# Optimization experiments

Measured on AMD Instinct MI355X. Metric: run time of the kernel, lower is better.

## Reference

```python
import jax, jax.numpy as jnp
import numpy as np

T, V, E, K, D, H, BERT = 4, 4096, 4096, 32, 8, 16, 768
CAT = H + BERT  # 784, second LSTM input size


def setup_inputs() -> dict:
    key = jax.random.key(0)
    ks = jax.random.split(key, 24)
    n = lambda k, s: jax.random.normal(k, s, dtype=jnp.float32) * 0.02
    return dict(
        prices=jax.random.normal(ks[0], (T, V, 1), dtype=jnp.float32),
        node_embs=jax.random.normal(ks[1], (T, E, BERT), dtype=jnp.float32),
        he_members=jax.random.randint(ks[2], (T, E, K), 0, V),
        vert_edges=jax.random.randint(ks[3], (T, V, D), 0, E),
        Wih_p=n(ks[4], (4 * H, 1)), Whh_p=n(ks[5], (4 * H, H)),
        bih_p=n(ks[6], (4 * H,)), bhh_p=n(ks[7], (4 * H,)),
        Wih_m=n(ks[8], (4 * H, CAT)), Whh_m=n(ks[9], (4 * H, H)),
        bih_m=n(ks[10], (4 * H,)), bhh_m=n(ks[11], (4 * H,)),
        vc_trans_w=n(ks[12], (K, K, H)), vc_trans_b=n(ks[13], (K, K)),
        vc_conv_w=n(ks[14], (K,)), vc_conv_b=n(ks[15], (1,)),
        ec_w1=n(ks[16], (CAT // 4, CAT)), ec_b1=n(ks[17], (CAT // 4,)),
        ec_w2=n(ks[18], (1, CAT // 4)), ec_b2=n(ks[19], (1,)),
        attn_in=n(ks[20], (H, H)), attn_out=n(ks[21], (H, 2 * H)),
        fc_w=n(ks[22], (2, H)), fc_b=n(ks[23], (2,)),
    )


def _lstm(x, Wih, Whh, bih, bhh):
    # x: (T, B, in) -> hidden states (T, B, H); PyTorch gate order i,f,g,o
    h0 = jnp.zeros((x.shape[1], Whh.shape[1]), x.dtype)
    b = bih + bhh

    def step(carry, xt):
        h, c = carry
        g = xt @ Wih.T + h @ Whh.T + b
        i, f, gg, o = jnp.split(g, 4, axis=-1)
        c = jax.nn.sigmoid(f) * c + jax.nn.sigmoid(i) * jnp.tanh(gg)
        h = jax.nn.sigmoid(o) * jnp.tanh(c)
        return (h, c), h

    _, hs = jax.lax.scan(step, (h0, h0), x)
    return hs


def reference(prices, node_embs, he_members, vert_edges,
              Wih_p, Whh_p, bih_p, bhh_p,
              Wih_m, Whh_m, bih_m, bhh_m,
              vc_trans_w, vc_trans_b, vc_conv_w, vc_conv_b,
              ec_w1, ec_b1, ec_w2, ec_b2,
              attn_in, attn_out, fc_w, fc_b):
    # price LSTM over lookback window: (T, V, 1) -> (T, V, H)
    new_prices = _lstm(prices, Wih_p, Whh_p, bih_p, bhh_p)

    # --- VertexConv (DHGNN): gather member price embeddings per hyperedge ---
    # reg[t,e,k] = new_prices[t, he_members[t,e,k]]  -> (T, E, K, H)
    reg = jax.vmap(lambda p, idx: p[idx])(new_prices, he_members)
    # grouped Conv1d(k, k*k, dim_in, groups=k): row i of multiplier depends on feat i
    mult = jnp.einsum('tekd,kjd->tekj', reg, vc_trans_w) + vc_trans_b
    mult = jax.nn.softmax(mult, axis=-1)                     # (T,E,K,K)
    trans = jnp.einsum('tekj,tejd->tekd', mult, reg)         # (T,E,K,H)
    he_emb = jnp.einsum('tekd,k->ted', trans, vc_conv_w) + vc_conv_b  # (T,E,H)

    # concat hyperedge emb with article embedding -> (T, E, 784)
    he_cat = jnp.concatenate([he_emb, node_embs], axis=-1)

    # --- EdgeConv: per-vertex attention over its D adjacent hyperedges ---
    ft = jax.vmap(lambda h, idx: h[idx])(he_cat, vert_edges)  # (T,V,D,CAT)
    s = jax.nn.relu(ft @ ec_w1.T + ec_b1) @ ec_w2.T + ec_b2   # (T,V,D,1)
    w = jax.nn.softmax(s, axis=2)
    hg = jnp.sum(w * ft, axis=2)                              # (T,V,CAT) == scatter into hg_tensor

    # second LSTM + residual with price embeddings
    lstm_out = _lstm(hg, Wih_m, Whh_m, bih_m, bhh_m)          # (T,V,H)
    la = lstm_out + new_prices

    # torchnlp 'general' Attention: query = last step, context = all steps
    q = la[-1] @ attn_in.T                                    # (V,H)
    ctx = jnp.transpose(la, (1, 0, 2))                        # (V,T,H)
    aw = jax.nn.softmax(jnp.einsum('vd,vtd->vt', q, ctx), axis=-1)
    mix = jnp.einsum('vt,vtd->vd', aw, ctx)
    attn = jnp.tanh(jnp.concatenate([mix, q], axis=-1) @ attn_out.T)  # (V,H)

    # final classifier (dropout identity in eval)
    return attn @ fc_w.T + fc_b                               # (V,2)
```

## Files before the change

### kernel.cpp

```cpp
#include <hip/hip_runtime.h>
#include <hip/hip_bf16.h>
#include <math.h>

#define TT 4
#define VV 4096
#define EE 4096
#define KK 32
#define DD 8
#define HH 16
#define BERTD 768
#define CATD 784
#define NH 196
#define NTOT 260
#define KPB 800
#define NPB 288
#define LDB 808

typedef __bf16 bf16x8 __attribute__((ext_vector_type(8)));
typedef float  f32x4  __attribute__((ext_vector_type(4)));

__device__ __forceinline__ float sigmoidf_(float x){ return 1.0f/(1.0f+expf(-x)); }
__device__ __forceinline__ unsigned short f2bf(float f){
  __bf16 h = (__bf16)f;
  return __builtin_bit_cast(unsigned short, h);
}
__device__ __forceinline__ float bf2f(unsigned short u){
  unsigned int x = ((unsigned int)u) << 16;
  return __builtin_bit_cast(float, x);
}
__device__ __forceinline__ uint4 pack8(float4 a, float4 b){
  uint4 u;
  u.x = (unsigned)f2bf(a.x) | ((unsigned)f2bf(a.y) << 16);
  u.y = (unsigned)f2bf(a.z) | ((unsigned)f2bf(a.w) << 16);
  u.z = (unsigned)f2bf(b.x) | ((unsigned)f2bf(b.y) << 16);
  u.w = (unsigned)f2bf(b.z) | ((unsigned)f2bf(b.w) << 16);
  return u;
}

__global__ __launch_bounds__(256) void kP(
    const float* __restrict__ prices,
    const float* __restrict__ Wih, const float* __restrict__ Whh,
    const float* __restrict__ bih, const float* __restrict__ bhh,
    float* __restrict__ np_out,
    const float* __restrict__ w1, const float* __restrict__ wm,
    unsigned short* __restrict__ Bbf,
    const float* __restrict__ tw, unsigned short* __restrict__ twbf,
    float* __restrict__ esc,
    const float* __restrict__ node, unsigned short* __restrict__ Abf){
  int b = blockIdx.x;
  int tid = threadIdx.x;
  if (b < 256){
    int lane = tid & 15;
    int v    = (b*256 + tid) >> 4;
    float W[4][16], wih[4], bb[4];
#pragma unroll
    for (int gi=0; gi<4; ++gi){
      int j = gi*16 + lane;
      const float4* wr = reinterpret_cast<const float4*>(&Whh[j*16]);
      float4 w0=wr[0], w1v=wr[1], w2v=wr[2], w3v=wr[3];
      W[gi][0]=w0.x; W[gi][1]=w0.y; W[gi][2]=w0.z; W[gi][3]=w0.w;
      W[gi][4]=w1v.x; W[gi][5]=w1v.y; W[gi][6]=w1v.z; W[gi][7]=w1v.w;
      W[gi][8]=w2v.x; W[gi][9]=w2v.y; W[gi][10]=w2v.z; W[gi][11]=w2v.w;
      W[gi][12]=w3v.x; W[gi][13]=w3v.y; W[gi][14]=w3v.z; W[gi][15]=w3v.w;
      wih[gi] = Wih[j];
      bb[gi]  = bih[j] + bhh[j];
    }
    float h = 0.f, c = 0.f;
    for (int t=0; t<TT; ++t){
      float x = prices[t*VV + v];
      float a0 = fmaf(x, wih[0], bb[0]);
      float a1 = fmaf(x, wih[1], bb[1]);
      float a2 = fmaf(x, wih[2], bb[2]);
      float a3 = fmaf(x, wih[3], bb[3]);
#pragma unroll
      for (int d=0; d<16; ++d){
        float hb = __shfl(h, d, 16);
        a0 = fmaf(hb, W[0][d], a0);
        a1 = fmaf(hb, W[1][d], a1);
        a2 = fmaf(hb, W[2][d], a2);
        a3 = fmaf(hb, W[3][d], a3);
      }
      float ig = sigmoidf_(a0);
      float fg = sigmoidf_(a1);
      float gg = tanhf(a2);
      float og = sigmoidf_(a3);
      c = fmaf(fg, c, ig*gg);
      h = og * tanhf(c);
      np_out[(size_t)(t*VV+v)*16 + lane] = h;
    }
  } else if (b < 544){
    int n = b - 256;
    const float* src = nullptr;
    if (n < NH)        src = &w1[(size_t)n*CATD];
    else if (n < NTOT) src = &wm[(size_t)(n-NH)*CATD];
    for (int kx = tid; kx < KPB; kx += 256){
      float v = (src != nullptr && kx < CATD) ? src[kx] : 0.f;
      Bbf[(size_t)n*KPB + kx] = f2bf(v);
    }
  } else if (b < 546){
    int base = (b - 544) * 512;
#pragma unroll
    for (int rr = 0; rr < 2; ++rr){
      int r = base + tid*2 + rr;
      const float* s = &tw[(size_t)r*16];
#pragma unroll
      for (int d = 0; d < 16; ++d) twbf[(size_t)r*16 + d] = f2bf(s[d]);
    }
  } else if (b < 562){
    int idx = ((b - 546)*256 + tid)*4;
    float4 z = make_float4(0.f,0.f,0.f,0.f);
    *reinterpret_cast<float4*>(&esc[idx]) = z;
  } else {
    int row = (b - 562)*16 + (tid >> 4);
    int c0  = (tid & 15) * 48;
    const float* src = &node[(size_t)row*BERTD + c0];
    unsigned short* dst = &Abf[(size_t)row*KPB + 16 + c0];
#pragma unroll
    for (int cc = 0; cc < 6; ++cc){
      float4 f0 = *reinterpret_cast<const float4*>(&src[cc*8]);
      float4 f1 = *reinterpret_cast<const float4*>(&src[cc*8+4]);
      *reinterpret_cast<uint4*>(&dst[cc*8]) = pack8(f0, f1);
    }
    if ((tid & 15) == 15){
      uint4 z = {0,0,0,0};
      unsigned short* zp = &Abf[(size_t)row*KPB + 784];
      *reinterpret_cast<uint4*>(&zp[0]) = z;
      *reinterpret_cast<uint4*>(&zp[8]) = z;
    }
  }
}

__global__ __launch_bounds__(256) void k2_fused(
    const float* __restrict__ np, const int* __restrict__ mem,
    const unsigned short* __restrict__ twbf, const float* __restrict__ tb,
    const float* __restrict__ cw, const float* __restrict__ cb,
    unsigned short* __restrict__ Abf){
  __shared__ unsigned short s_reg[32*16*16];
  __shared__ float s_wsumP[4][16][32];
  __shared__ int   s_mem[512];
  int tid = threadIdx.x;
  int te0 = blockIdx.x * 16;
  for (int i = tid; i < 512; i += 256) s_mem[i] = mem[(size_t)te0*32 + i];
  __syncthreads();
  for (int p = tid; p < 512; p += 256){
    int gte = p & 15, gk = p >> 4;
    int t   = (te0 + gte) >> 12;
    int vid = s_mem[gte*32 + gk];
    const float4* src = reinterpret_cast<const float4*>(&np[((size_t)(t*VV) + vid)*16]);
    float4 f0 = src[0], f1 = src[1], f2 = src[2], f3 = src[3];
    uint4* dst = reinterpret_cast<uint4*>(&s_reg[(gk*16 + gte)*16]);
    dst[0] = pack8(f0, f1);
    dst[1] = pack8(f2, f3);
  }
  __syncthreads();
  int l = tid & 63;
  int w = tid >> 6;
  int lj = l & 15;
  int lg = l >> 4;
  float w0acc[4] = {0.f,0.f,0.f,0.f};
  float w1acc[4] = {0.f,0.f,0.f,0.f};
#pragma unroll
  for (int kk = 0; kk < 8; ++kk){
    int k = w*8 + kk;
    bf16x8 af = 0, b0 = 0, b1v = 0;
    if (l < 32){
      af  = *reinterpret_cast<const bf16x8*>(&s_reg[(k*16 + lj)*16 + lg*8]);
      b0  = *reinterpret_cast<const bf16x8*>(&twbf[((size_t)k*32 + lj)*16 + lg*8]);
      b1v = *reinterpret_cast<const bf16x8*>(&twbf[((size_t)k*32 + 16 + lj)*16 + lg*8]);
    }
    float tb0 = tb[k*32 + lj];
    float tb1 = tb[k*32 + 16 + lj];
    f32x4 c0 = {tb0, tb0, tb0, tb0};
    f32x4 c1 = {tb1, tb1, tb1, tb1};
    f32x4 s0 = __builtin_amdgcn_mfma_f32_16x16x32_bf16(af, b0,  c0, 0, 0, 0);
    f32x4 s1 = __builtin_amdgcn_mfma_f32_16x16x32_bf16(af, b1v, c1, 0, 0, 0);
    float cwk = cw[k];
#pragma unroll
    for (int i = 0; i < 4; ++i){
      float v0 = s0[i], v1 = s1[i];
      float m = fmaxf(v0, v1);
#pragma unroll
      for (int off = 1; off < 16; off <<= 1) m = fmaxf(m, __shfl_xor(m, off, 16));
      float e0 = expf(v0 - m), e1 = expf(v1 - m);
      float sm = e0 + e1;
#pragma unroll
      for (int off = 1; off < 16; off <<= 1) sm += __shfl_xor(sm, off, 16);
      float f = cwk / sm;
      w0acc[i] = fmaf(e0, f, w0acc[i]);
      w1acc[i] = fmaf(e1, f, w1acc[i]);
    }
  }
#pragma unroll
  for (int i = 0; i < 4; ++i){
    int ter = lg*4 + i;
    s_wsumP[w][ter][lj]      = w0acc[i];
    s_wsumP[w][ter][16 + lj] = w1acc[i];
  }
  __syncthreads();
  int te = tid >> 4, d = tid & 15;
  float he = cb[0];
#pragma unroll
  for (int j = 0; j < 32; ++j){
    float ws = s_wsumP[0][te][j] + s_wsumP[1][te][j]
             + s_wsumP[2][te][j] + s_wsumP[3][te][j];
    he = fmaf(ws, bf2f(s_reg[(j*16 + te)*16 + d]), he);
  }
  Abf[((size_t)(te0 + te))*KPB + d] = f2bf(he);
}

__global__ __launch_bounds__(256) void k3_gemm_mfma(
    const unsigned short* __restrict__ Abf,
    const unsigned short* __restrict__ Bbf, const float* __restrict__ b1,
    const float* __restrict__ w2, float* __restrict__ esc,
    float* __restrict__ C_pe){
  __shared__ unsigned short Bs[48*LDB];
  int tid = threadIdx.x;
  int bid = blockIdx.x;
  int group = bid / 48;
  int within = bid - group*48;
  int nc  = within >> 3;
  int mbr = within & 7;
  int mb  = group*8 + mbr;
  for (int i = tid; i < 4800; i += 256){
    int r = i / 100, c = i - r*100;
    *reinterpret_cast<uint4*>(&Bs[r*LDB + c*8]) =
      *reinterpret_cast<const uint4*>(&Bbf[(size_t)(nc*48 + r)*KPB + c*8]);
  }
  __syncthreads();
  int l = tid & 63, w = tid >> 6;
  int lr = l & 15, ls = l >> 4;
  int m0 = mb*128 + w*32;
  const unsigned short* a0p = &Abf[(size_t)(m0 + lr)*KPB];
  const unsigned short* a1p = a0p + (size_t)16*KPB;
  const unsigned short* bbase = &Bs[lr*LDB + ls*8];
  f32x4 acc[2][3] = {};
#pragma unroll
  for (int s = 0; s < 25; ++s){
    bf16x8 af0 = *reinterpret_cast<const bf16x8*>(&a0p[s*32 + ls*8]);
    bf16x8 af1 = *reinterpret_cast<const bf16x8*>(&a1p[s*32 + ls*8]);
#pragma unroll
    for (int j = 0; j < 3; ++j){
      bf16x8 bfv = *reinterpret_cast<const bf16x8*>(&bbase[j*16*LDB + s*32]);
      acc[0][j] = __builtin_amdgcn_mfma_f32_16x16x32_bf16(af0, bfv, acc[0][j], 0, 0, 0);
      acc[1][j] = __builtin_amdgcn_mfma_f32_16x16x32_bf16(af1, bfv, acc[1][j], 0, 0, 0);
    }
  }
  float p[2][4] = {{0.f,0.f,0.f,0.f},{0.f,0.f,0.f,0.f}};
#pragma unroll
  for (int j = 0; j < 3; ++j){
    int n = nc*48 + j*16 + lr;
    bool hid = (n < NH);
    float b1n = hid ? b1[n] : 0.f;
    float w2n = hid ? w2[n] : 0.f;
#pragma unroll
    for (int i = 0; i < 2; ++i){
#pragma unroll
      for (int q = 0; q < 4; ++q){
        float v = acc[i][j][q];
        if (hid){
          p[i][q] += fmaxf(v + b1n, 0.f) * w2n;
        } else if (n < NTOT){
          int m = m0 + i*16 + ls*4 + q;
          C_pe[(size_t)m*64 + (n - NH)] = v;
        }
      }
    }
  }
  if (nc*48 < NH){
#pragma unroll
    for (int i = 0; i < 2; ++i){
#pragma unroll
      for (int q = 0; q < 4; ++q){
        float v = p[i][q];
#pragma unroll
        for (int off = 1; off < 16; off <<= 1) v += __shfl_xor(v, off, 16);
        if (lr == 0){
          int m = m0 + i*16 + ls*4 + q;
          atomicAdd(&esc[m], v);
        }
      }
    }
  }
}

__global__ __launch_bounds__(256) void k456(
    const int* __restrict__ ve, const float* __restrict__ esc,
    const float* __restrict__ C_pe, const float* __restrict__ np,
    const float* __restrict__ Whh, const float* __restrict__ bih,
    const float* __restrict__ bhh,
    const float* __restrict__ ain, const float* __restrict__ aout,
    const float* __restrict__ fcw, const float* __restrict__ fcb,
    float* __restrict__ out){
  __shared__ float s_ain[16*17];
  __shared__ float s_aout[16*33];
  __shared__ float s_fc[32];
  __shared__ float s_fcb[2];
  int tid = threadIdx.x;
  { int j = tid >> 4, d = tid & 15; s_ain[j*17+d] = ain[tid]; }
  for (int i = tid; i < 512; i += 256){ int j = i >> 5, d = i & 31; s_aout[j*33+d] = aout[i]; }
  if (tid < 32) s_fc[tid] = fcw[tid];
  if (tid < 2)  s_fcb[tid] = fcb[tid];
  int lane = tid & 15;
  int v = (blockIdx.x*256 + tid) >> 4;
  float W[4][16], b[4];
#pragma unroll
  for (int gi=0; gi<4; ++gi){
    int j = gi*16 + lane;
    const float4* wr = reinterpret_cast<const float4*>(&Whh[j*16]);
    float4 w0=wr[0], w1=wr[1], w2=wr[2], w3=wr[3];
    W[gi][0]=w0.x; W[gi][1]=w0.y; W[gi][2]=w0.z; W[gi][3]=w0.w;
    W[gi][4]=w1.x; W[gi][5]=w1.y; W[gi][6]=w1.z; W[gi][7]=w1.w;
    W[gi][8]=w2.x; W[gi][9]=w2.y; W[gi][10]=w2.z; W[gi][11]=w2.w;
    W[gi][12]=w3.x; W[gi][13]=w3.y; W[gi][14]=w3.z; W[gi][15]=w3.w;
    b[gi] = bih[j] + bhh[j];
  }
  __syncthreads();
  float h = 0.f, c = 0.f;
  float la0, la1, la2, la3;
#pragma unroll
  for (int t=0; t<TT; ++t){
    const int* vp = &ve[((size_t)(t*VV) + v)*8];
    int e[8]; float wv[8];
    float mx = -1e30f;
#pragma unroll
    for (int d = 0; d < 8; ++d){
      e[d] = vp[d];
      wv[d] = esc[(t << 12) + e[d]];
      mx = fmaxf(mx, wv[d]);
    }
    float s = 0.f;
#pragma unroll
    for (int d = 0; d < 8; ++d){ wv[d] = expf(wv[d]-mx); s += wv[d]; }
    float inv = 1.f/s;
#pragma unroll
    for (int d = 0; d < 8; ++d) wv[d] *= inv;
    float g0 = b[0], g1 = b[1], g2 = b[2], g3 = b[3];
#pragma unroll
    for (int d = 0; d < 8; ++d){
      const float* cp = &C_pe[(size_t)((t << 12) + e[d])*64];
      g0 = fmaf(wv[d], cp[lane],      g0);
      g1 = fmaf(wv[d], cp[16 + lane], g1);
      g2 = fmaf(wv[d], cp[32 + lane], g2);
      g3 = fmaf(wv[d], cp[48 + lane], g3);
    }
#pragma unroll
    for (int d=0; d<16; ++d){
      float hb = __shfl(h, d, 16);
      g0 = fmaf(hb, W[0][d], g0);
      g1 = fmaf(hb, W[1][d], g1);
      g2 = fmaf(hb, W[2][d], g2);
      g3 = fmaf(hb, W[3][d], g3);
    }
    float ig = sigmoidf_(g0);
    float fg = sigmoidf_(g1);
    float gg = tanhf(g2);
    float og = sigmoidf_(g3);
    c = fmaf(fg, c, ig*gg);
    h = og * tanhf(c);
    float la = h + np[(size_t)(t*VV+v)*16 + lane];
    if (t == 0) la0 = la; else if (t == 1) la1 = la;
    else if (t == 2) la2 = la; else la3 = la;
  }
  float q = 0.f;
#pragma unroll
  for (int d=0; d<16; ++d){
    float bb = __shfl(la3, d, 16);
    q = fmaf(bb, s_ain[lane*17+d], q);
  }
  float aw0 = q*la0, aw1 = q*la1, aw2 = q*la2, aw3 = q*la3;
#pragma unroll
  for (int off=1; off<16; off<<=1){
    aw0 += __shfl_xor(aw0, off, 16);
    aw1 += __shfl_xor(aw1, off, 16);
    aw2 += __shfl_xor(aw2, off, 16);
    aw3 += __shfl_xor(aw3, off, 16);
  }
  float mx = fmaxf(fmaxf(aw0,aw1), fmaxf(aw2,aw3));
  aw0 = expf(aw0-mx); aw1 = expf(aw1-mx); aw2 = expf(aw2-mx); aw3 = expf(aw3-mx);
  float inv = 1.f/(aw0+aw1+aw2+aw3);
  float mix = (aw0*la0 + aw1*la1 + aw2*la2 + aw3*la3) * inv;
  float a = 0.f;
#pragma unroll
  for (int d=0; d<16; ++d){
    float m  = __shfl(mix, d, 16);
    float qq = __shfl(q,  d, 16);
    a = fmaf(m,  s_aout[lane*33+d],    a);
    a = fmaf(qq, s_aout[lane*33+16+d], a);
  }
  float at = tanhf(a);
  float p0 = at * s_fc[lane];
  float p1 = at * s_fc[16+lane];
#pragma unroll
  for (int off=1; off<16; off<<=1){
    p0 += __shfl_xor(p0, off, 16);
    p1 += __shfl_xor(p1, off, 16);
  }
  if (lane == 0){
    out[(size_t)v*2 + 0] = p0 + s_fcb[0];
    out[(size_t)v*2 + 1] = p1 + s_fcb[1];
  }
}

extern "C" void kernel_launch(void* const* d_in, const int* in_sizes, int n_in,
                              void* d_out, int out_size, void* d_ws, size_t ws_size,
                              hipStream_t stream){
  const float* prices = (const float*)d_in[0];
  const float* node   = (const float*)d_in[1];
  const int*   mem    = (const int*)d_in[2];
  const int*   ve     = (const int*)d_in[3];
  const float* Wih_p  = (const float*)d_in[4];
  const float* Whh_p  = (const float*)d_in[5];
  const float* bih_p  = (const float*)d_in[6];
  const float* bhh_p  = (const float*)d_in[7];
  const float* Wih_m  = (const float*)d_in[8];
  const float* Whh_m  = (const float*)d_in[9];
  const float* bih_m  = (const float*)d_in[10];
  const float* bhh_m  = (const float*)d_in[11];
  const float* tw     = (const float*)d_in[12];
  const float* tb     = (const float*)d_in[13];
  const float* cw     = (const float*)d_in[14];
  const float* cb     = (const float*)d_in[15];
  const float* w1     = (const float*)d_in[16];
  const float* b1     = (const float*)d_in[17];
  const float* w2     = (const float*)d_in[18];
  const float* ain    = (const float*)d_in[20];
  const float* aout   = (const float*)d_in[21];
  const float* fcw    = (const float*)d_in[22];
  const float* fcb    = (const float*)d_in[23];

  float* np_buf = (float*)d_ws;
  float* esc    = np_buf + (size_t)TT*VV*HH;
  float* C_pe   = esc    + (size_t)TT*EE;
  unsigned short* Bbf  = (unsigned short*)(C_pe + (size_t)TT*EE*64);
  unsigned short* twbf = Bbf + (size_t)NPB*KPB;
  unsigned short* Abf  = twbf + (size_t)1024*16;

  kP<<<1586, 256, 0, stream>>>(prices, Wih_p, Whh_p, bih_p, bhh_p, np_buf,
                               w1, Wih_m, Bbf, tw, twbf, esc, node, Abf);
  k2_fused<<<(TT*EE)/16, 256, 0, stream>>>(np_buf, mem, twbf, tb, cw, cb, Abf);
  k3_gemm_mfma<<<768, 256, 0, stream>>>(Abf, Bbf, b1, w2, esc, C_pe);
  k456<<<(VV*16)/256, 256, 0, stream>>>(ve, esc, C_pe, np_buf, Whh_m, bih_m, bhh_m,
                                        ain, aout, fcw, fcb, (float*)d_out);
}
```

Baseline: 211.9 us.

## Pre-swizzle A and B bf16 operands into MFMA fragment order

The node-embedding A matrix and the w1/Wih_m B matrix are now written by the prep kernel directly in per-16-row, per-K-step MFMA fragment order, so each lane's 8-element fragment is contiguous. The GEMM then issues fully coalesced 16-byte loads for A from global memory and copies B into shared memory linearly, with no padded stride. The k2 kernel's write of the hyperedge embedding columns is remapped to the same layout. This removes the strided row loads (800-element row pitch) in the GEMM, at the cost of more index arithmetic in the prep kernel and coupling every producer to the fragment layout.

```diff
diff --git a/kernel.cpp b/kernel.cpp
--- a/kernel.cpp
+++ b/kernel.cpp
@@ -12,9 +12,8 @@
 #define CATD 784
 #define NH 196
 #define NTOT 260
-#define KPB 800
+#define NSTEP 25
 #define NPB 288
-#define LDB 808
 
 typedef __bf16 bf16x8 __attribute__((ext_vector_type(8)));
 typedef float  f32x4  __attribute__((ext_vector_type(4)));
@@ -36,6 +35,7 @@
   u.w = (unsigned)f2bf(b.z) | ((unsigned)f2bf(b.w) << 16);
   return u;
 }
+
 
 __global__ __launch_bounds__(256) void kP(
     const float* __restrict__ prices,
@@ -49,9 +49,29 @@
     const float* __restrict__ node, unsigned short* __restrict__ Abf){
   int b = blockIdx.x;
   int tid = threadIdx.x;
-  if (b < 256){
+  if (b < 1024){
+    int f16 = b;
+    for (int i = tid; i < 1600; i += 256){
+      int s = i >> 6, l = i & 63;
+      int lr = l & 15, ls = l >> 4;
+      int k = s*32 + ls*8;
+      if (s == 0 && ls < 2) continue;
+      uint4* dst = reinterpret_cast<uint4*>(&Abf[((size_t)(f16*NSTEP + s)*64 + l)*8]);
+      if (k >= CATD){
+        uint4 z = {0,0,0,0};
+        *dst = z;
+      } else {
+        int row = f16*16 + lr;
+        const float* src = &node[(size_t)row*BERTD + (k - 16)];
+        float4 f0 = *reinterpret_cast<const float4*>(&src[0]);
+        float4 f1 = *reinterpret_cast<const float4*>(&src[4]);
+        *dst = pack8(f0, f1);
+      }
+    }
+  } else if (b < 1280){
+    int bb2 = b - 1024;
     int lane = tid & 15;
-    int v    = (b*256 + tid) >> 4;
+    int v    = (bb2*256 + tid) >> 4;
     float W[4][16], wih[4], bb[4];
 #pragma unroll
     for (int gi=0; gi<4; ++gi){
@@ -88,17 +108,27 @@
       h = og * tanhf(c);
       np_out[(size_t)(t*VV+v)*16 + lane] = h;
     }
-  } else if (b < 544){
-    int n = b - 256;
-    const float* src = nullptr;
-    if (n < NH)        src = &w1[(size_t)n*CATD];
-    else if (n < NTOT) src = &wm[(size_t)(n-NH)*CATD];
-    for (int kx = tid; kx < KPB; kx += 256){
-      float v = (src != nullptr && kx < CATD) ? src[kx] : 0.f;
-      Bbf[(size_t)n*KPB + kx] = f2bf(v);
-    }
-  } else if (b < 546){
-    int base = (b - 544) * 512;
+  } else if (b < 1298){
+    int n16 = b - 1280;
+    for (int i = tid; i < 1600; i += 256){
+      int s = i >> 6, l = i & 63;
+      int lr = l & 15, ls = l >> 4;
+      int n = n16*16 + lr;
+      int k = s*32 + ls*8;
+      uint4* dst = reinterpret_cast<uint4*>(&Bbf[((size_t)(n16*NSTEP + s)*64 + l)*8]);
+      if (n < NTOT && k < CATD){
+        const float* src = (n < NH) ? &w1[(size_t)n*CATD + k]
+                                    : &wm[(size_t)(n-NH)*CATD + k];
+        float4 f0 = *reinterpret_cast<const float4*>(&src[0]);
+        float4 f1 = *reinterpret_cast<const float4*>(&src[4]);
+        *dst = pack8(f0, f1);
+      } else {
+        uint4 z = {0,0,0,0};
+        *dst = z;
+      }
+    }
+  } else if (b < 1300){
+    int base = (b - 1298) * 512;
 #pragma unroll
     for (int rr = 0; rr < 2; ++rr){
       int r = base + tid*2 + rr;
@@ -106,27 +136,10 @@
 #pragma unroll
       for (int d = 0; d < 16; ++d) twbf[(size_t)r*16 + d] = f2bf(s[d]);
     }
-  } else if (b < 562){
-    int idx = ((b - 546)*256 + tid)*4;
+  } else {
+    int idx = ((b - 1300)*256 + tid)*4;
     float4 z = make_float4(0.f,0.f,0.f,0.f);
     *reinterpret_cast<float4*>(&esc[idx]) = z;
-  } else {
-    int row = (b - 562)*16 + (tid >> 4);
-    int c0  = (tid & 15) * 48;
-    const float* src = &node[(size_t)row*BERTD + c0];
-    unsigned short* dst = &Abf[(size_t)row*KPB + 16 + c0];
-#pragma unroll
-    for (int cc = 0; cc < 6; ++cc){
-      float4 f0 = *reinterpret_cast<const float4*>(&src[cc*8]);
-      float4 f1 = *reinterpret_cast<const float4*>(&src[cc*8+4]);
-      *reinterpret_cast<uint4*>(&dst[cc*8]) = pack8(f0, f1);
-    }
-    if ((tid & 15) == 15){
-      uint4 z = {0,0,0,0};
-      unsigned short* zp = &Abf[(size_t)row*KPB + 784];
-      *reinterpret_cast<uint4*>(&zp[0]) = z;
-      *reinterpret_cast<uint4*>(&zp[8]) = z;
-    }
   }
 }
 
@@ -205,7 +218,8 @@
              + s_wsumP[2][te][j] + s_wsumP[3][te][j];
     he = fmaf(ws, bf2f(s_reg[(j*16 + te)*16 + d]), he);
   }
-  Abf[((size_t)(te0 + te))*KPB + d] = f2bf(he);
+  int f16 = blockIdx.x;
+  Abf[((size_t)(f16*NSTEP + 0)*64 + (d >> 3)*16 + te)*8 + (d & 7)] = f2bf(he);
 }
 
 __global__ __launch_bounds__(256) void k3_gemm_mfma(
@@ -213,7 +227,7 @@
     const unsigned short* __restrict__ Bbf, const float* __restrict__ b1,
     const float* __restrict__ w2, float* __restrict__ esc,
     float* __restrict__ C_pe){
-  __shared__ unsigned short Bs[48*LDB];
+  __shared__ unsigned short Bs[3*NSTEP*64*8];
   int tid = threadIdx.x;
   int bid = blockIdx.x;
   int group = bid / 48;
@@ -221,26 +235,25 @@
   int nc  = within >> 3;
   int mbr = within & 7;
   int mb  = group*8 + mbr;
-  for (int i = tid; i < 4800; i += 256){
-    int r = i / 100, c = i - r*100;
-    *reinterpret_cast<uint4*>(&Bs[r*LDB + c*8]) =
-      *reinterpret_cast<const uint4*>(&Bbf[(size_t)(nc*48 + r)*KPB + c*8]);
+  {
+    const uint4* src = reinterpret_cast<const uint4*>(&Bbf[(size_t)(nc*3)*NSTEP*64*8]);
+    uint4* dst = reinterpret_cast<uint4*>(Bs);
+    for (int i = tid; i < 4800; i += 256) dst[i] = src[i];
   }
   __syncthreads();
   int l = tid & 63, w = tid >> 6;
   int lr = l & 15, ls = l >> 4;
   int m0 = mb*128 + w*32;
-  const unsigned short* a0p = &Abf[(size_t)(m0 + lr)*KPB];
-  const unsigned short* a1p = a0p + (size_t)16*KPB;
-  const unsigned short* bbase = &Bs[lr*LDB + ls*8];
+  int f16 = (m0 >> 4);
+  const unsigned short* a0p = &Abf[(size_t)f16*NSTEP*512];
   f32x4 acc[2][3] = {};
 #pragma unroll
-  for (int s = 0; s < 25; ++s){
-    bf16x8 af0 = *reinterpret_cast<const bf16x8*>(&a0p[s*32 + ls*8]);
-    bf16x8 af1 = *reinterpret_cast<const bf16x8*>(&a1p[s*32 + ls*8]);
+  for (int s = 0; s < NSTEP; ++s){
+    bf16x8 af0 = *reinterpret_cast<const bf16x8*>(&a0p[(s*64 + l)*8]);
+    bf16x8 af1 = *reinterpret_cast<const bf16x8*>(&a0p[((NSTEP + s)*64 + l)*8]);
 #pragma unroll
     for (int j = 0; j < 3; ++j){
-      bf16x8 bfv = *reinterpret_cast<const bf16x8*>(&bbase[j*16*LDB + s*32]);
+      bf16x8 bfv = *reinterpret_cast<const bf16x8*>(&Bs[((j*NSTEP + s)*64 + l)*8]);
       acc[0][j] = __builtin_amdgcn_mfma_f32_16x16x32_bf16(af0, bfv, acc[0][j], 0, 0, 0);
       acc[1][j] = __builtin_amdgcn_mfma_f32_16x16x32_bf16(af1, bfv, acc[1][j], 0, 0, 0);
     }
@@ -432,10 +445,10 @@
   float* esc    = np_buf + (size_t)TT*VV*HH;
   float* C_pe   = esc    + (size_t)TT*EE;
   unsigned short* Bbf  = (unsigned short*)(C_pe + (size_t)TT*EE*64);
-  unsigned short* twbf = Bbf + (size_t)NPB*KPB;
+  unsigned short* twbf = Bbf + (size_t)18*NSTEP*512;
   unsigned short* Abf  = twbf + (size_t)1024*16;
 
-  kP<<<1586, 256, 0, stream>>>(prices, Wih_p, Whh_p, bih_p, bhh_p, np_buf,
+  kP<<<1316, 256, 0, stream>>>(prices, Wih_p, Whh_p, bih_p, bhh_p, np_buf,
                                w1, Wih_m, Bbf, tw, twbf, esc, node, Abf);
   k2_fused<<<(TT*EE)/16, 256, 0, stream>>>(np_buf, mem, twbf, tb, cw, cb, Abf);
   k3_gemm_mfma<<<768, 256, 0, stream>>>(Abf, Bbf, b1, w2, esc, C_pe);
```

Result: faster. 206.0 us (-2.8%).
